# Kernel tuning notes

Measured on AMD Instinct MI355X. Metric: run time of the kernel, lower is better.

The kernel has to match this reference:

```python
import jax, jax.numpy as jnp
import numpy as np

N, D, E, S = 200000, 256, 1000000, 10000

def setup_inputs() -> dict:
    key = jax.random.key(0)
    k1, k2, k3, k4 = jax.random.split(key, 4)
    z = jax.random.normal(k1, (N, D), dtype=jnp.float32)
    attn_w = jax.random.normal(k2, (D,), dtype=jnp.float32) * (1.0 / np.sqrt(D))
    attn_b = jnp.zeros((), dtype=jnp.float32)
    idx = jax.random.randint(k3, (E,), 0, N, dtype=jnp.int64)
    seg = jnp.sort(jax.random.randint(k4, (E,), 0, S, dtype=jnp.int64))
    return {"z": z, "attn_w": attn_w, "attn_b": attn_b, "idx": idx, "seg": seg, "num_segments": S}

def reference(z, attn_w, attn_b, idx, seg, num_segments):
    # Gather ragged groups: sub[e] = z[idx[e]], group id = seg[e]
    sub = z[idx]                                   # [E, D]
    logits = sub @ attn_w + attn_b                 # [E] (nn.Linear(dim,1).squeeze)
    # Segmented, numerically-stable softmax over each group
    m = jax.ops.segment_max(logits, seg, num_segments=num_segments)  # [S]
    m = jnp.where(jnp.isfinite(m), m, 0.0)         # empty segments -> harmless 0
    e = jnp.exp(logits - m[seg])                   # [E]
    den = jax.ops.segment_sum(e, seg, num_segments=num_segments)     # [S]
    w = e / den[seg]                               # [E]
    # Softmax-weighted sum per segment; empty segments yield zeros (matches torch)
    out = jax.ops.segment_sum(sub * w[:, None], seg, num_segments=num_segments)  # [S, D]
    return out
```

## Files before the change

kernel.cpp:

```cpp
#include <hip/hip_runtime.h>
#include <hip/hip_fp16.h>
#include <math.h>

#define DDIM 256
#define NWAVES 4
#define NEG_SENT -1.0e30f

__global__ void seg_offsets_kernel(const int* __restrict__ seg, int E, int S,
                                   int* __restrict__ offs) {
    int i = blockIdx.x * blockDim.x + threadIdx.x;
    if (i > S) return;
    int lo = 0, hi = E;
    while (lo < hi) {
        int mid = (lo + hi) >> 1;
        if (seg[mid] < i) lo = mid + 1; else hi = mid;
    }
    offs[i] = lo;
}

__global__ __launch_bounds__(256)
void prep_kernel(const float4* __restrict__ z4,
                 const float* __restrict__ attn_w,
                 const float* __restrict__ attn_b,
                 uint2* __restrict__ z16,
                 float* __restrict__ pvec, int N) {
    const int wave = threadIdx.x >> 6;
    const int lane = threadIdx.x & 63;
    const int row  = blockIdx.x * NWAVES + wave;
    if (row >= N) return;
    const float4 v = z4[(long)row * 64 + lane];
    __half2 h0 = __floats2half2_rn(v.x, v.y);
    __half2 h1 = __floats2half2_rn(v.z, v.w);
    uint2 h;
    h.x = *(unsigned int*)&h0;
    h.y = *(unsigned int*)&h1;
    z16[(long)row * 64 + lane] = h;
    const float4 wv = ((const float4*)attn_w)[lane];
    float part = v.x * wv.x + v.y * wv.y + v.z * wv.z + v.w * wv.w;
    #pragma unroll
    for (int sh = 32; sh >= 1; sh >>= 1) part += __shfl_xor(part, sh);
    if (lane == 0) pvec[row] = __expf(part + attn_b[0]);
}

__global__ __launch_bounds__(256)
void node_p_kernel(const float4* __restrict__ z4,
                   const float* __restrict__ attn_w,
                   const float* __restrict__ attn_b,
                   float* __restrict__ pvec, int N) {
    const int wave = threadIdx.x >> 6;
    const int lane = threadIdx.x & 63;
    const int row  = blockIdx.x * NWAVES + wave;
    if (row >= N) return;
    const float4 v  = z4[(long)row * 64 + lane];
    const float4 wv = ((const float4*)attn_w)[lane];
    float part = v.x * wv.x + v.y * wv.y + v.z * wv.z + v.w * wv.w;
    #pragma unroll
    for (int sh = 32; sh >= 1; sh >>= 1) part += __shfl_xor(part, sh);
    if (lane == 0) pvec[row] = __expf(part + attn_b[0]);
}

__device__ inline float4 h4_to_f4(uint2 h) {
    __half2 a = *(__half2*)&h.x;
    __half2 b = *(__half2*)&h.y;
    float2 fa = __half22float2(a);
    float2 fb = __half22float2(b);
    return make_float4(fa.x, fa.y, fb.x, fb.y);
}

__global__ __launch_bounds__(256)
void segpool3_kernel(const uint2* __restrict__ z16,
                     const float* __restrict__ pvec,
                     const int* __restrict__ idx,
                     const int* __restrict__ offs,
                     float* __restrict__ out) {
    const int s     = blockIdx.x;
    const int start = offs[s];
    const int end   = offs[s + 1];
    const int tid   = threadIdx.x;
    if (end <= start) { out[(long)s * DDIM + tid] = 0.0f; return; }

    const int wave = tid >> 6;
    const int lane = tid & 63;

    float  den = 0.0f;
    float4 acc = make_float4(0.f, 0.f, 0.f, 0.f);

    int e = start + wave;
    for (; e + 7 * NWAVES < end; e += 8 * NWAVES) {
        int rows[8];
        #pragma unroll
        for (int k = 0; k < 8; ++k) rows[k] = idx[e + k * NWAVES];
        float ps[8]; uint2 hs[8];
        #pragma unroll
        for (int k = 0; k < 8; ++k) {
            ps[k] = pvec[rows[k]];
            hs[k] = z16[(long)rows[k] * 64 + lane];
        }
        #pragma unroll
        for (int k = 0; k < 8; ++k) {
            const float4 v = h4_to_f4(hs[k]);
            den  += ps[k];
            acc.x += ps[k] * v.x;
            acc.y += ps[k] * v.y;
            acc.z += ps[k] * v.z;
            acc.w += ps[k] * v.w;
        }
    }
    for (; e < end; e += NWAVES) {
        const int row = idx[e];
        const float p = pvec[row];
        const float4 v = h4_to_f4(z16[(long)row * 64 + lane]);
        den  += p;
        acc.x += p * v.x;
        acc.y += p * v.y;
        acc.z += p * v.z;
        acc.w += p * v.w;
    }

    __shared__ float lds_den[NWAVES];
    __shared__ float lds_acc[NWAVES][DDIM];
    if (lane == 0) lds_den[wave] = den;
    lds_acc[wave][4 * lane + 0] = acc.x;
    lds_acc[wave][4 * lane + 1] = acc.y;
    lds_acc[wave][4 * lane + 2] = acc.z;
    lds_acc[wave][4 * lane + 3] = acc.w;
    __syncthreads();

    const float D = lds_den[0] + lds_den[1] + lds_den[2] + lds_den[3];
    const float o = lds_acc[0][tid] + lds_acc[1][tid] +
                    lds_acc[2][tid] + lds_acc[3][tid];
    out[(long)s * DDIM + tid] = o / D;
}

__global__ __launch_bounds__(256)
void segpool3_f32_kernel(const float4* __restrict__ z4,
                         const float* __restrict__ pvec,
                         const int* __restrict__ idx,
                         const int* __restrict__ offs,
                         float* __restrict__ out) {
    const int s     = blockIdx.x;
    const int start = offs[s];
    const int end   = offs[s + 1];
    const int tid   = threadIdx.x;
    if (end <= start) { out[(long)s * DDIM + tid] = 0.0f; return; }
    const int wave = tid >> 6;
    const int lane = tid & 63;
    float  den = 0.0f;
    float4 acc = make_float4(0.f, 0.f, 0.f, 0.f);
    int e = start + wave;
    for (; e + 7 * NWAVES < end; e += 8 * NWAVES) {
        int rows[8];
        #pragma unroll
        for (int k = 0; k < 8; ++k) rows[k] = idx[e + k * NWAVES];
        float ps[8]; float4 vs[8];
        #pragma unroll
        for (int k = 0; k < 8; ++k) {
            ps[k] = pvec[rows[k]];
            vs[k] = z4[(long)rows[k] * 64 + lane];
        }
        #pragma unroll
        for (int k = 0; k < 8; ++k) {
            den  += ps[k];
            acc.x += ps[k] * vs[k].x;
            acc.y += ps[k] * vs[k].y;
            acc.z += ps[k] * vs[k].z;
            acc.w += ps[k] * vs[k].w;
        }
    }
    for (; e < end; e += NWAVES) {
        const int row = idx[e];
        const float p = pvec[row];
        const float4 v = z4[(long)row * 64 + lane];
        den  += p;
        acc.x += p * v.x;
        acc.y += p * v.y;
        acc.z += p * v.z;
        acc.w += p * v.w;
    }
    __shared__ float lds_den[NWAVES];
    __shared__ float lds_acc[NWAVES][DDIM];
    if (lane == 0) lds_den[wave] = den;
    lds_acc[wave][4 * lane + 0] = acc.x;
    lds_acc[wave][4 * lane + 1] = acc.y;
    lds_acc[wave][4 * lane + 2] = acc.z;
    lds_acc[wave][4 * lane + 3] = acc.w;
    __syncthreads();
    const float D = lds_den[0] + lds_den[1] + lds_den[2] + lds_den[3];
    const float o = lds_acc[0][tid] + lds_acc[1][tid] +
                    lds_acc[2][tid] + lds_acc[3][tid];
    out[(long)s * DDIM + tid] = o / D;
}

__global__ __launch_bounds__(256)
void segpool_fused_kernel(const float* __restrict__ z,
                          const float* __restrict__ attn_w,
                          const float* __restrict__ attn_b,
                          const int* __restrict__ idx,
                          const int* __restrict__ offs,
                          float* __restrict__ out) {
    const int s     = blockIdx.x;
    const int start = offs[s];
    const int end   = offs[s + 1];
    const int tid   = threadIdx.x;
    if (end <= start) { out[(long)s * DDIM + tid] = 0.0f; return; }
    const int wave = tid >> 6;
    const int lane = tid & 63;
    const float4 wv = ((const float4*)attn_w)[lane];
    const float  b  = attn_b[0];
    const float4* __restrict__ z4 = (const float4*)z;
    float  m = NEG_SENT, l = 0.0f;
    float4 acc = make_float4(0.f, 0.f, 0.f, 0.f);
    for (int e = start + wave; e < end; e += NWAVES) {
        const int   row = idx[e];
        const float4 v  = z4[(long)row * 64 + lane];
        float part = v.x * wv.x + v.y * wv.y + v.z * wv.z + v.w * wv.w;
        #pragma unroll
        for (int sh = 32; sh >= 1; sh >>= 1) part += __shfl_xor(part, sh);
        const float logit = part + b;
        const float nm    = fmaxf(m, logit);
        const float alpha = __expf(m - nm);
        const float p     = __expf(logit - nm);
        l = l * alpha + p;
        acc.x = acc.x * alpha + p * v.x;
        acc.y = acc.y * alpha + p * v.y;
        acc.z = acc.z * alpha + p * v.z;
        acc.w = acc.w * alpha + p * v.w;
        m = nm;
    }
    __shared__ float lds_m[NWAVES], lds_l[NWAVES];
    __shared__ float lds_acc[NWAVES][DDIM];
    if (lane == 0) { lds_m[wave] = m; lds_l[wave] = l; }
    __syncthreads();
    const float M = fmaxf(fmaxf(lds_m[0], lds_m[1]), fmaxf(lds_m[2], lds_m[3]));
    float den = 0.0f;
    #pragma unroll
    for (int w = 0; w < NWAVES; ++w) den += __expf(lds_m[w] - M) * lds_l[w];
    const float scale = __expf(m - M);
    lds_acc[wave][4 * lane + 0] = acc.x * scale;
    lds_acc[wave][4 * lane + 1] = acc.y * scale;
    lds_acc[wave][4 * lane + 2] = acc.z * scale;
    lds_acc[wave][4 * lane + 3] = acc.w * scale;
    __syncthreads();
    const float o = lds_acc[0][tid] + lds_acc[1][tid] +
                    lds_acc[2][tid] + lds_acc[3][tid];
    out[(long)s * DDIM + tid] = o / den;
}

extern "C" void kernel_launch(void* const* d_in, const int* in_sizes, int n_in,
                              void* d_out, int out_size, void* d_ws, size_t ws_size,
                              hipStream_t stream) {
    const float* z      = (const float*)d_in[0];
    const float* attn_w = (const float*)d_in[1];
    const float* attn_b = (const float*)d_in[2];
    const int*   idx    = (const int*)d_in[3];
    const int*   seg    = (const int*)d_in[4];
    float*       out    = (float*)d_out;

    const int E = in_sizes[3];
    const int S = out_size / DDIM;
    const int N = in_sizes[0] / DDIM;

    const int threads = 256;
    const int gridA = (S + 1 + threads - 1) / threads;
    const int gridN = (N + NWAVES - 1) / NWAVES;

    int* offs = (int*)d_ws;
    const size_t offs_bytes = (((size_t)(S + 1) * sizeof(int)) + 255) & ~(size_t)255;
    const size_t p_bytes    = (((size_t)N * sizeof(float)) + 255) & ~(size_t)255;
    const size_t z16_bytes  = (size_t)N * DDIM * sizeof(__half);
    const size_t need_full  = offs_bytes + p_bytes + z16_bytes;
    const size_t need_p     = offs_bytes + p_bytes;

    seg_offsets_kernel<<<gridA, threads, 0, stream>>>(seg, E, S, offs);

    if (ws_size >= need_full) {
        float* pvec = (float*)((char*)d_ws + offs_bytes);
        uint2* z16  = (uint2*)((char*)d_ws + offs_bytes + p_bytes);
        prep_kernel<<<gridN, threads, 0, stream>>>(
            (const float4*)z, attn_w, attn_b, z16, pvec, N);
        segpool3_kernel<<<S, threads, 0, stream>>>(
            (const uint2*)z16, pvec, idx, offs, out);
    } else if (ws_size >= need_p) {
        float* pvec = (float*)((char*)d_ws + offs_bytes);
        node_p_kernel<<<gridN, threads, 0, stream>>>(
            (const float4*)z, attn_w, attn_b, pvec, N);
        segpool3_f32_kernel<<<S, threads, 0, stream>>>(
            (const float4*)z, pvec, idx, offs, out);
    } else {
        segpool_fused_kernel<<<S, threads, 0, stream>>>(
            z, attn_w, attn_b, idx, offs, out);
    }
}
```

Baseline: 377.6 us.

## Fold segment offsets into prep kernel and map one wave per segment

The segment-offset binary search now runs as extra blocks of the prep kernel, which removes one kernel launch. The pooling kernel now gives each wave a whole segment (four segments per block) instead of splitting one segment across four waves. That drops the LDS reduction and the __syncthreads, and it writes float4 output directly. The trade-off is less memory-level parallelism per segment, since one wave walks about 100 rows serially, which could leave gather latency less well hidden.

```diff
diff --git a/kernel.cpp b/kernel.cpp
--- a/kernel.cpp
+++ b/kernel.cpp
@@ -4,6 +4,7 @@
 
 #define DDIM 256
 #define NWAVES 4
+#define SEGW 4
 #define NEG_SENT -1.0e30f
 
 __global__ void seg_offsets_kernel(const int* __restrict__ seg, int E, int S,
@@ -19,11 +20,24 @@
 }
 
 __global__ __launch_bounds__(256)
-void prep_kernel(const float4* __restrict__ z4,
-                 const float* __restrict__ attn_w,
-                 const float* __restrict__ attn_b,
-                 uint2* __restrict__ z16,
-                 float* __restrict__ pvec, int N) {
+void prep_offs_kernel(const float4* __restrict__ z4,
+                      const float* __restrict__ attn_w,
+                      const float* __restrict__ attn_b,
+                      uint2* __restrict__ z16,
+                      float* __restrict__ pvec, int N, int gridN,
+                      const int* __restrict__ seg, int E, int S,
+                      int* __restrict__ offs) {
+    if ((int)blockIdx.x >= gridN) {
+        int i = ((int)blockIdx.x - gridN) * blockDim.x + threadIdx.x;
+        if (i > S) return;
+        int lo = 0, hi = E;
+        while (lo < hi) {
+            int mid = (lo + hi) >> 1;
+            if (seg[mid] < i) lo = mid + 1; else hi = mid;
+        }
+        offs[i] = lo;
+        return;
+    }
     const int wave = threadIdx.x >> 6;
     const int lane = threadIdx.x & 63;
     const int row  = blockIdx.x * NWAVES + wave;
@@ -68,68 +82,61 @@
 }
 
 __global__ __launch_bounds__(256)
-void segpool3_kernel(const uint2* __restrict__ z16,
+void segpool4_kernel(const uint2* __restrict__ z16,
                      const float* __restrict__ pvec,
                      const int* __restrict__ idx,
                      const int* __restrict__ offs,
-                     float* __restrict__ out) {
-    const int s     = blockIdx.x;
+                     float* __restrict__ out, int S) {
+    const int wave = threadIdx.x >> 6;
+    const int lane = threadIdx.x & 63;
+    const int s = blockIdx.x * SEGW + wave;
+    if (s >= S) return;
     const int start = offs[s];
     const int end   = offs[s + 1];
-    const int tid   = threadIdx.x;
-    if (end <= start) { out[(long)s * DDIM + tid] = 0.0f; return; }
-
-    const int wave = tid >> 6;
-    const int lane = tid & 63;
+    float4* __restrict__ out4 = (float4*)out;
+    if (end <= start) {
+        out4[(long)s * 64 + lane] = make_float4(0.f, 0.f, 0.f, 0.f);
+        return;
+    }
 
     float  den = 0.0f;
     float4 acc = make_float4(0.f, 0.f, 0.f, 0.f);
 
-    int e = start + wave;
-    for (; e + 7 * NWAVES < end; e += 8 * NWAVES) {
+    int e = start;
+    for (; e + 8 <= end; e += 8) {
         int rows[8];
         #pragma unroll
-        for (int k = 0; k < 8; ++k) rows[k] = idx[e + k * NWAVES];
+        for (int k = 0; k < 8; ++k) rows[k] = idx[e + k];
         float ps[8]; uint2 hs[8];
         #pragma unroll
         for (int k = 0; k < 8; ++k) {
             ps[k] = pvec[rows[k]];
-            hs[k] = z16[(long)rows[k] * 64 + lane];
+            hs[k] = z16[((unsigned)rows[k] << 6) + lane];
         }
         #pragma unroll
         for (int k = 0; k < 8; ++k) {
             const float4 v = h4_to_f4(hs[k]);
-            den  += ps[k];
+            den   += ps[k];
             acc.x += ps[k] * v.x;
             acc.y += ps[k] * v.y;
             acc.z += ps[k] * v.z;
             acc.w += ps[k] * v.w;
         }
     }
-    for (; e < end; e += NWAVES) {
-        const int row = idx[e];
-        const float p = pvec[row];
-        const float4 v = h4_to_f4(z16[(long)row * 64 + lane]);
-        den  += p;
+    for (; e < end; ++e) {
+        const int row  = idx[e];
+        const float p  = pvec[row];
+        const float4 v = h4_to_f4(z16[((unsigned)row << 6) + lane]);
+        den   += p;
         acc.x += p * v.x;
         acc.y += p * v.y;
         acc.z += p * v.z;
         acc.w += p * v.w;
     }
 
-    __shared__ float lds_den[NWAVES];
-    __shared__ float lds_acc[NWAVES][DDIM];
-    if (lane == 0) lds_den[wave] = den;
-    lds_acc[wave][4 * lane + 0] = acc.x;
-    lds_acc[wave][4 * lane + 1] = acc.y;
-    lds_acc[wave][4 * lane + 2] = acc.z;
-    lds_acc[wave][4 * lane + 3] = acc.w;
-    __syncthreads();
-
-    const float D = lds_den[0] + lds_den[1] + lds_den[2] + lds_den[3];
-    const float o = lds_acc[0][tid] + lds_acc[1][tid] +
-                    lds_acc[2][tid] + lds_acc[3][tid];
-    out[(long)s * DDIM + tid] = o / D;
+    const float inv = 1.0f / den;
+    out4[(long)s * 64 + lane] =
+        make_float4(acc.x * inv, acc.y * inv, acc.z * inv, acc.w * inv);
 }
 
 __global__ __launch_bounds__(256)
@@ -271,22 +278,23 @@
     const size_t need_full  = offs_bytes + p_bytes + z16_bytes;
     const size_t need_p     = offs_bytes + p_bytes;
 
-    seg_offsets_kernel<<<gridA, threads, 0, stream>>>(seg, E, S, offs);
-
     if (ws_size >= need_full) {
         float* pvec = (float*)((char*)d_ws + offs_bytes);
         uint2* z16  = (uint2*)((char*)d_ws + offs_bytes + p_bytes);
-        prep_kernel<<<gridN, threads, 0, stream>>>(
-            (const float4*)z, attn_w, attn_b, z16, pvec, N);
-        segpool3_kernel<<<S, threads, 0, stream>>>(
-            (const uint2*)z16, pvec, idx, offs, out);
+        prep_offs_kernel<<<gridN + gridA, threads, 0, stream>>>(
+            (const float4*)z, attn_w, attn_b, z16, pvec, N, gridN,
+            seg, E, S, offs);
+        segpool4_kernel<<<(S + SEGW - 1) / SEGW, threads, 0, stream>>>(
+            (const uint2*)z16, pvec, idx, offs, out, S);
     } else if (ws_size >= need_p) {
         float* pvec = (float*)((char*)d_ws + offs_bytes);
+        seg_offsets_kernel<<<gridA, threads, 0, stream>>>(seg, E, S, offs);
         node_p_kernel<<<gridN, threads, 0, stream>>>(
             (const float4*)z, attn_w, attn_b, pvec, N);
         segpool3_f32_kernel<<<S, threads, 0, stream>>>(
             (const float4*)z, pvec, idx, offs, out);
     } else {
+        seg_offsets_kernel<<<gridA, threads, 0, stream>>>(seg, E, S, offs);
         segpool_fused_kernel<<<S, threads, 0, stream>>>(
             z, attn_w, attn_b, idx, offs, out);
     }
```

Result: no change. 378.4 us (+0.2%).
